# Kernel optimization log

Measured on AMD Instinct MI355X. Metric: run time of the kernel, lower is better.

Reference implementation:

```python
import jax, jax.numpy as jnp
import numpy as np

SIGMA = 0.1
B_PARAM = 1.0
EPS_NORM = 1e-12  # torch F.normalize eps
EPS_MIN = 1e-5


def setup_inputs() -> dict:
    key = jax.random.key(0)
    k1, k2 = jax.random.split(key)
    x = jax.random.normal(k1, (4, 64, 64, 64), dtype=jnp.float32)
    y = jax.random.normal(k2, (4, 64, 64, 64), dtype=jnp.float32)
    return {"x": x, "y": y}


def reference(x, y):
    B, C, H, W = x.shape
    N = H * W
    xf = x.reshape(B, C, N)
    yf = y.reshape(B, C, N)
    # F.normalize along channel dim (L2, eps-clamped denominator)
    xn = xf / jnp.maximum(jnp.linalg.norm(xf, axis=1, keepdims=True), EPS_NORM)
    yn = yf / jnp.maximum(jnp.linalg.norm(yf, axis=1, keepdims=True), EPS_NORM)
    xt = jnp.transpose(xn, (0, 2, 1))  # [B, N, C]
    yt = jnp.transpose(yn, (0, 2, 1))  # [B, N, C]
    x2 = jnp.sum(xt * xt, axis=-1, keepdims=True)          # [B, N, 1]
    y2 = jnp.sum(yt * yt, axis=-1)[:, None, :]             # [B, 1, N]
    d2 = x2 + y2 - 2.0 * jnp.einsum('bnc,bmc->bnm', xt, yt)  # [B, N, N]
    dist = jnp.sqrt(jnp.maximum(d2, 0.0))
    d_min = jnp.min(dist, axis=-1, keepdims=True)
    d_scaled = dist / (d_min + EPS_MIN)
    w = jnp.exp((B_PARAM - d_scaled) / SIGMA)
    cx = w / jnp.sum(w, axis=-1, keepdims=True)
    cx_max = jnp.max(cx, axis=-1)  # [B, N]
    return -jnp.log(jnp.mean(cx_max + EPS_MIN))
```

## Files before the change

### kernel.cpp

```cpp
#include <hip/hip_runtime.h>
#include <math.h>

constexpr int B_   = 4;
constexpr int C_   = 64;
constexpr int HW   = 4096;
constexpr int ROWS = B_ * HW;

constexpr float SIGMA    = 0.1f;
constexpr float EPS_MIN  = 1e-5f;
constexpr float EPS_NORM = 1e-12f;
constexpr float LOG2E    = 1.44269504088896340736f;

constexpr int XR  = 64;
constexpr int NW  = 16;
constexpr int YW  = HW / NW;
constexpr int SRW = 32;
constexpr int NSW = YW / SRW;

using short8  = __attribute__((ext_vector_type(8))) short;
using floatx4 = __attribute__((ext_vector_type(4))) float;

__device__ inline ushort f2bf(float f) {
    unsigned u = __float_as_uint(f);
    unsigned r = u + 0x7FFFu + ((u >> 16) & 1u);
    return (ushort)(r >> 16);
}

__global__ __launch_bounds__(256) void nrm_kernel(const float* __restrict__ x,
                                                  const float* __restrict__ y,
                                                  ushort* __restrict__ xn,
                                                  ushort* __restrict__ yn,
                                                  float* __restrict__ total) {
    int p = blockIdx.x * 256 + threadIdx.x;
    if (p == 0) *total = 0.0f;
    const float* src; ushort* dst; int q; float sgn;
    if (p < ROWS) { src = x; dst = xn; q = p; sgn = -2.0f; }
    else          { src = y; dst = yn; q = p - ROWS; sgn = 1.0f; }
    int b = q >> 12;
    int n = q & (HW - 1);
    const float* base = src + ((size_t)b * C_) * HW + n;
    float v[C_];
    float ss = 0.0f;
#pragma unroll
    for (int c = 0; c < C_; ++c) {
        v[c] = base[(size_t)c * HW];
        ss = fmaf(v[c], v[c], ss);
    }
    float scale = sgn / fmaxf(sqrtf(ss), EPS_NORM);
    short8* o = (short8*)(dst + (size_t)q * C_);
#pragma unroll
    for (int c8 = 0; c8 < C_ / 8; ++c8) {
        short8 pk;
#pragma unroll
        for (int j = 0; j < 8; ++j) pk[j] = (short)f2bf(v[c8 * 8 + j] * scale);
        o[c8] = pk;
    }
}

__global__ __launch_bounds__(1024, 4) void main_kernel(const ushort* __restrict__ xn,
                                                       const ushort* __restrict__ yn,
                                                       float* __restrict__ total) {
    __shared__ short8 stg[NW][2][SRW * 8];
    __shared__ float  red[NW][XR];
    __shared__ float  dmf[XR];

    const int tid  = threadIdx.x;
    const int wid  = tid >> 6;
    const int lane = tid & 63;
    const int lrow = lane & 15;
    const int kgrp = lane >> 4;

    const int blk   = blockIdx.x;
    const int b     = blk >> 6;
    const int nbase = (blk & 63) * XR;

    const ushort* xb = xn + (size_t)(b * HW + nbase) * C_;
    short8 xf0[4], xf1[4];
#pragma unroll
    for (int xt = 0; xt < 4; ++xt) {
        xf0[xt] = *(const short8*)(xb + (xt * 16 + lrow) * C_ + kgrp * 8);
        xf1[xt] = *(const short8*)(xb + (xt * 16 + lrow) * C_ + 32 + kgrp * 8);
    }

    const short8* yq = (const short8*)(yn + (size_t)(b * HW + wid * YW) * C_);
    const int wbase = (lane >> 3) * 8 + ((lane & 7) ^ (lane >> 3));

    short8 v[4];
    float m2[4] = {INFINITY, INFINITY, INFINITY, INFINITY};

#pragma unroll
    for (int g = 0; g < 4; ++g) v[g] = yq[g * 64 + lane];
#pragma unroll
    for (int g = 0; g < 4; ++g) stg[wid][0][g * 64 + wbase] = v[g];

    for (int s = 0; s < NSW; ++s) {
        int cur = s & 1;
        if (s + 1 < NSW) {
#pragma unroll
            for (int g = 0; g < 4; ++g) v[g] = yq[(s + 1) * 256 + g * 64 + lane];
        }
#pragma unroll
        for (int yt = 0; yt < 2; ++yt) {
            int p = yt * 16 + lrow, q = p & 7;
            short8 ya0 = stg[wid][cur][p * 8 + (kgrp ^ q)];
            short8 ya1 = stg[wid][cur][p * 8 + ((kgrp + 4) ^ q)];
#pragma unroll
            for (int xt = 0; xt < 4; ++xt) {
                floatx4 acc = {2.0f, 2.0f, 2.0f, 2.0f};
                acc = __builtin_amdgcn_mfma_f32_16x16x32_bf16(ya0, xf0[xt], acc, 0, 0, 0);
                acc = __builtin_amdgcn_mfma_f32_16x16x32_bf16(ya1, xf1[xt], acc, 0, 0, 0);
                m2[xt] = fminf(m2[xt],
                         fminf(fminf(acc[0], acc[1]), fminf(acc[2], acc[3])));
            }
        }
        if (s + 1 < NSW) {
#pragma unroll
            for (int g = 0; g < 4; ++g) stg[wid][cur ^ 1][g * 64 + wbase] = v[g];
        }
    }

#pragma unroll
    for (int off = 16; off < 64; off <<= 1)
#pragma unroll
        for (int xt = 0; xt < 4; ++xt)
            m2[xt] = fminf(m2[xt], __shfl_xor(m2[xt], off));
    if (kgrp == 0)
#pragma unroll
        for (int xt = 0; xt < 4; ++xt) red[wid][xt * 16 + lrow] = m2[xt];
    __syncthreads();
    if (tid < XR) {
        float m = red[0][tid];
#pragma unroll
        for (int w = 1; w < NW; ++w) m = fminf(m, red[w][tid]);
        dmf[tid] = sqrtf(fmaxf(m, 0.0f));
    }
    __syncthreads();

    float kk2[4], c02[4];
#pragma unroll
    for (int xt = 0; xt < 4; ++xt) {
        float dm = dmf[xt * 16 + lrow];
        kk2[xt] = LOG2E / (SIGMA * (dm + EPS_MIN));
        c02[xt] = dm * kk2[xt];
    }

    float s2[4] = {0.0f, 0.0f, 0.0f, 0.0f};
#pragma unroll
    for (int g = 0; g < 4; ++g) v[g] = yq[g * 64 + lane];
#pragma unroll
    for (int g = 0; g < 4; ++g) stg[wid][0][g * 64 + wbase] = v[g];

    for (int s = 0; s < NSW; ++s) {
        int cur = s & 1;
        if (s + 1 < NSW) {
#pragma unroll
            for (int g = 0; g < 4; ++g) v[g] = yq[(s + 1) * 256 + g * 64 + lane];
        }
#pragma unroll
        for (int yt = 0; yt < 2; ++yt) {
            int p = yt * 16 + lrow, q = p & 7;
            short8 ya0 = stg[wid][cur][p * 8 + (kgrp ^ q)];
            short8 ya1 = stg[wid][cur][p * 8 + ((kgrp + 4) ^ q)];
#pragma unroll
            for (int xt = 0; xt < 4; ++xt) {
                floatx4 acc = {2.0f, 2.0f, 2.0f, 2.0f};
                acc = __builtin_amdgcn_mfma_f32_16x16x32_bf16(ya0, xf0[xt], acc, 0, 0, 0);
                acc = __builtin_amdgcn_mfma_f32_16x16x32_bf16(ya1, xf1[xt], acc, 0, 0, 0);
#pragma unroll
                for (int r = 0; r < 4; ++r) {
                    float d = __builtin_amdgcn_sqrtf(acc[r]);
                    s2[xt] += __builtin_amdgcn_exp2f(fmaf(-kk2[xt], d, c02[xt]));
                }
            }
        }
        if (s + 1 < NSW) {
#pragma unroll
            for (int g = 0; g < 4; ++g) stg[wid][cur ^ 1][g * 64 + wbase] = v[g];
        }
    }

#pragma unroll
    for (int off = 16; off < 64; off <<= 1)
#pragma unroll
        for (int xt = 0; xt < 4; ++xt)
            s2[xt] += __shfl_xor(s2[xt], off);
    if (kgrp == 0)
#pragma unroll
        for (int xt = 0; xt < 4; ++xt) red[wid][xt * 16 + lrow] = s2[xt];
    __syncthreads();

    if (tid < 64) {
        float Ssum = red[0][tid];
#pragma unroll
        for (int w = 1; w < NW; ++w) Ssum += red[w][tid];
        float acc = __builtin_amdgcn_rcpf(Ssum) + EPS_MIN;
#pragma unroll
        for (int off = 32; off > 0; off >>= 1) acc += __shfl_down(acc, off);
        if (tid == 0) atomicAdd(total, acc);
    }
}

__global__ void final_kernel(const float* __restrict__ total,
                             float* __restrict__ out) {
    out[0] = -logf(total[0] / (float)ROWS);
}

extern "C" void kernel_launch(void* const* d_in, const int* in_sizes, int n_in,
                              void* d_out, int out_size, void* d_ws, size_t ws_size,
                              hipStream_t stream) {
    const float* x = (const float*)d_in[0];
    const float* y = (const float*)d_in[1];
    float* out = (float*)d_out;

    char* ws = (char*)d_ws;
    size_t nrm_bytes = (size_t)ROWS * C_ * sizeof(ushort);
    ushort* xn    = (ushort*)(ws);
    ushort* yn    = (ushort*)(ws + nrm_bytes);
    float*  total = (float*)(ws + 2 * nrm_bytes);

    hipLaunchKernelGGL(nrm_kernel, dim3(2 * ROWS / 256), dim3(256), 0, stream,
                       x, y, xn, yn, total);
    hipLaunchKernelGGL(main_kernel, dim3(ROWS / XR), dim3(1024), 0, stream,
                       xn, yn, total);
    hipLaunchKernelGGL(final_kernel, dim3(1), dim3(1), 0, stream, total, out);
}
```

Baseline: 93.29 us.

## Fuse normalize, distance and final kernels into one cooperative launch

Merges the normalization, main distance/softmax pass and final log into a single cooperative kernel separated by grid-wide syncs, removing two kernel launches and their gaps. Normalization is respread so 8 threads share one row, with a shuffle reduction of the sum of squares. The min and exp accumulations are lightly reordered. It relies on all 256 blocks of 1024 threads being co-resident, and grid.sync adds its own barrier cost.

```diff
diff --git a/kernel.cpp b/kernel.cpp
--- a/kernel.cpp
+++ b/kernel.cpp
@@ -1,5 +1,8 @@
 #include <hip/hip_runtime.h>
+#include <hip/hip_cooperative_groups.h>
 #include <math.h>
+
+namespace cg = cooperative_groups;
 
 constexpr int B_   = 4;
 constexpr int C_   = 64;
@@ -26,40 +29,10 @@
     return (ushort)(r >> 16);
 }
 
-__global__ __launch_bounds__(256) void nrm_kernel(const float* __restrict__ x,
-                                                  const float* __restrict__ y,
-                                                  ushort* __restrict__ xn,
-                                                  ushort* __restrict__ yn,
-                                                  float* __restrict__ total) {
-    int p = blockIdx.x * 256 + threadIdx.x;
-    if (p == 0) *total = 0.0f;
-    const float* src; ushort* dst; int q; float sgn;
-    if (p < ROWS) { src = x; dst = xn; q = p; sgn = -2.0f; }
-    else          { src = y; dst = yn; q = p - ROWS; sgn = 1.0f; }
-    int b = q >> 12;
-    int n = q & (HW - 1);
-    const float* base = src + ((size_t)b * C_) * HW + n;
-    float v[C_];
-    float ss = 0.0f;
-#pragma unroll
-    for (int c = 0; c < C_; ++c) {
-        v[c] = base[(size_t)c * HW];
-        ss = fmaf(v[c], v[c], ss);
-    }
-    float scale = sgn / fmaxf(sqrtf(ss), EPS_NORM);
-    short8* o = (short8*)(dst + (size_t)q * C_);
-#pragma unroll
-    for (int c8 = 0; c8 < C_ / 8; ++c8) {
-        short8 pk;
-#pragma unroll
-        for (int j = 0; j < 8; ++j) pk[j] = (short)f2bf(v[c8 * 8 + j] * scale);
-        o[c8] = pk;
-    }
-}
-
-__global__ __launch_bounds__(1024, 4) void main_kernel(const ushort* __restrict__ xn,
-                                                       const ushort* __restrict__ yn,
-                                                       float* __restrict__ total) {
+__global__ __launch_bounds__(1024, 4)
+void fused_kernel(const float* __restrict__ x, const float* __restrict__ y,
+                  ushort* __restrict__ xn, ushort* __restrict__ yn,
+                  float* __restrict__ total, float* __restrict__ out) {
     __shared__ short8 stg[NW][2][SRW * 8];
     __shared__ float  red[NW][XR];
     __shared__ float  dmf[XR];
@@ -69,8 +42,38 @@
     const int lane = tid & 63;
     const int lrow = lane & 15;
     const int kgrp = lane >> 4;
-
-    const int blk   = blockIdx.x;
+    const int blk  = blockIdx.x;
+
+    cg::grid_group grid = cg::this_grid();
+
+    {
+        int g   = blk * 1024 + tid;
+        int p   = g >> 3;
+        int oct = g & 7;
+        if (g == 0) *total = 0.0f;
+        const float* src; ushort* dst; int q; float sgn;
+        if (p < ROWS) { src = x; dst = xn; q = p; sgn = -2.0f; }
+        else          { src = y; dst = yn; q = p - ROWS; sgn = 1.0f; }
+        int b = q >> 12;
+        int n = q & (HW - 1);
+        const float* base = src + (size_t)(b * C_) * HW + n;
+        float v[8];
+        float ss = 0.0f;
+#pragma unroll
+        for (int j = 0; j < 8; ++j) {
+            v[j] = base[(oct * 8 + j) * HW];
+            ss = fmaf(v[j], v[j], ss);
+        }
+#pragma unroll
+        for (int o = 1; o < 8; o <<= 1) ss += __shfl_xor(ss, o);
+        float scale = sgn / fmaxf(sqrtf(ss), EPS_NORM);
+        short8 pk;
+#pragma unroll
+        for (int j = 0; j < 8; ++j) pk[j] = (short)f2bf(v[j] * scale);
+        ((short8*)(dst + (size_t)q * C_))[oct] = pk;
+    }
+    grid.sync();
+
     const int b     = blk >> 6;
     const int nbase = (blk & 63) * XR;
 
@@ -109,8 +112,8 @@
                 floatx4 acc = {2.0f, 2.0f, 2.0f, 2.0f};
                 acc = __builtin_amdgcn_mfma_f32_16x16x32_bf16(ya0, xf0[xt], acc, 0, 0, 0);
                 acc = __builtin_amdgcn_mfma_f32_16x16x32_bf16(ya1, xf1[xt], acc, 0, 0, 0);
-                m2[xt] = fminf(m2[xt],
-                         fminf(fminf(acc[0], acc[1]), fminf(acc[2], acc[3])));
+                m2[xt] = fminf(fminf(fminf(acc[0], acc[1]), acc[2]),
+                               fminf(acc[3], m2[xt]));
             }
         }
         if (s + 1 < NSW) {
@@ -166,11 +169,14 @@
                 floatx4 acc = {2.0f, 2.0f, 2.0f, 2.0f};
                 acc = __builtin_amdgcn_mfma_f32_16x16x32_bf16(ya0, xf0[xt], acc, 0, 0, 0);
                 acc = __builtin_amdgcn_mfma_f32_16x16x32_bf16(ya1, xf1[xt], acc, 0, 0, 0);
-#pragma unroll
-                for (int r = 0; r < 4; ++r) {
-                    float d = __builtin_amdgcn_sqrtf(acc[r]);
-                    s2[xt] += __builtin_amdgcn_exp2f(fmaf(-kk2[xt], d, c02[xt]));
-                }
+                float d0 = __builtin_amdgcn_sqrtf(acc[0]);
+                float d1 = __builtin_amdgcn_sqrtf(acc[1]);
+                float d2 = __builtin_amdgcn_sqrtf(acc[2]);
+                float d3 = __builtin_amdgcn_sqrtf(acc[3]);
+                s2[xt] += __builtin_amdgcn_exp2f(fmaf(-kk2[xt], d0, c02[xt]));
+                s2[xt] += __builtin_amdgcn_exp2f(fmaf(-kk2[xt], d1, c02[xt]));
+                s2[xt] += __builtin_amdgcn_exp2f(fmaf(-kk2[xt], d2, c02[xt]));
+                s2[xt] += __builtin_amdgcn_exp2f(fmaf(-kk2[xt], d3, c02[xt]));
             }
         }
         if (s + 1 < NSW) {
@@ -198,11 +204,9 @@
         for (int off = 32; off > 0; off >>= 1) acc += __shfl_down(acc, off);
         if (tid == 0) atomicAdd(total, acc);
     }
-}
-
-__global__ void final_kernel(const float* __restrict__ total,
-                             float* __restrict__ out) {
-    out[0] = -logf(total[0] / (float)ROWS);
+
+    grid.sync();
+    if (blk == 0 && tid == 0) out[0] = -logf(total[0] / (float)ROWS);
 }
 
 extern "C" void kernel_launch(void* const* d_in, const int* in_sizes, int n_in,
@@ -218,9 +222,8 @@
     ushort* yn    = (ushort*)(ws + nrm_bytes);
     float*  total = (float*)(ws + 2 * nrm_bytes);
 
-    hipLaunchKernelGGL(nrm_kernel, dim3(2 * ROWS / 256), dim3(256), 0, stream,
-                       x, y, xn, yn, total);
-    hipLaunchKernelGGL(main_kernel, dim3(ROWS / XR), dim3(1024), 0, stream,
-                       xn, yn, total);
-    hipLaunchKernelGGL(final_kernel, dim3(1), dim3(1), 0, stream, total, out);
+    void* args[] = { (void*)&x, (void*)&y, (void*)&xn, (void*)&yn,
+                     (void*)&total, (void*)&out };
+    hipLaunchCooperativeKernel((const void*)fused_kernel, dim3(256), dim3(1024),
+                               args, 0, stream);
 }
```

Measured after the change: 148.6 us. 1.59x slower.

## Load Y tiles straight into LDS and fuse the final reduction kernel

Applied to the files above, without the earlier changes.

The y-tile staging now uses global_load_lds to copy 16-byte chunks straight from global memory into each wave's LDS double buffer, ordered by vmcnt waits. This replaces the register round trip and the ds_write. The XOR bank swizzle moves into the normalization kernel's store, so the raw copy still lands in conflict-free order. The separate single-thread final kernel is removed: the last block, found with an atomic counter, computes the log. This saves one launch but adds a threadfence and atomic tail to every block.

```diff
diff --git a/kernel.cpp b/kernel.cpp
--- a/kernel.cpp
+++ b/kernel.cpp
@@ -5,6 +5,7 @@
 constexpr int C_   = 64;
 constexpr int HW   = 4096;
 constexpr int ROWS = B_ * HW;
+constexpr int GRID = 256;
 
 constexpr float SIGMA    = 0.1f;
 constexpr float EPS_MIN  = 1e-5f;
@@ -26,19 +27,28 @@
     return (ushort)(r >> 16);
 }
 
+__device__ inline void gload16(const ushort* g, void* lds) {
+    __builtin_amdgcn_global_load_lds(
+        (const __attribute__((address_space(1))) void*)g,
+        (__attribute__((address_space(3))) void*)lds, 16, 0, 0);
+}
+
+#define WAIT_VMCNT(n) asm volatile("s_waitcnt vmcnt(" #n ")" ::: "memory")
+
 __global__ __launch_bounds__(256) void nrm_kernel(const float* __restrict__ x,
                                                   const float* __restrict__ y,
                                                   ushort* __restrict__ xn,
                                                   ushort* __restrict__ yn,
-                                                  float* __restrict__ total) {
+                                                  float* __restrict__ total,
+                                                  unsigned* __restrict__ cnt) {
     int p = blockIdx.x * 256 + threadIdx.x;
-    if (p == 0) *total = 0.0f;
-    const float* src; ushort* dst; int q; float sgn;
-    if (p < ROWS) { src = x; dst = xn; q = p; sgn = -2.0f; }
-    else          { src = y; dst = yn; q = p - ROWS; sgn = 1.0f; }
+    if (p == 0) { *total = 0.0f; *cnt = 0u; }
+    const float* src; ushort* dst; int q; float sgn; bool isy;
+    if (p < ROWS) { src = x; dst = xn; q = p; sgn = -2.0f; isy = false; }
+    else          { src = y; dst = yn; q = p - ROWS; sgn = 1.0f; isy = true; }
     int b = q >> 12;
     int n = q & (HW - 1);
-    const float* base = src + ((size_t)b * C_) * HW + n;
+    const float* base = src + (size_t)(b * C_) * HW + n;
     float v[C_];
     float ss = 0.0f;
 #pragma unroll
@@ -48,18 +58,21 @@
     }
     float scale = sgn / fmaxf(sqrtf(ss), EPS_NORM);
     short8* o = (short8*)(dst + (size_t)q * C_);
+    int sw = isy ? (n & 7) : 0;
 #pragma unroll
     for (int c8 = 0; c8 < C_ / 8; ++c8) {
         short8 pk;
 #pragma unroll
         for (int j = 0; j < 8; ++j) pk[j] = (short)f2bf(v[c8 * 8 + j] * scale);
-        o[c8] = pk;
+        o[c8 ^ sw] = pk;
     }
 }
 
 __global__ __launch_bounds__(1024, 4) void main_kernel(const ushort* __restrict__ xn,
                                                        const ushort* __restrict__ yn,
-                                                       float* __restrict__ total) {
+                                                       float* __restrict__ total,
+                                                       unsigned* __restrict__ cnt,
+                                                       float* __restrict__ out) {
     __shared__ short8 stg[NW][2][SRW * 8];
     __shared__ float  red[NW][XR];
     __shared__ float  dmf[XR];
@@ -82,23 +95,23 @@
         xf1[xt] = *(const short8*)(xb + (xt * 16 + lrow) * C_ + 32 + kgrp * 8);
     }
 
-    const short8* yq = (const short8*)(yn + (size_t)(b * HW + wid * YW) * C_);
-    const int wbase = (lane >> 3) * 8 + ((lane & 7) ^ (lane >> 3));
-
-    short8 v[4];
+    const ushort* yb = yn + (size_t)(b * HW + wid * YW) * C_ + lane * 8;
+
+#define ISSUE(s, buf) do {                                              \
+        const ushort* gp_ = yb + (size_t)(s) * SRW * C_;                \
+        _Pragma("unroll")                                               \
+        for (int g_ = 0; g_ < 4; ++g_)                                  \
+            gload16(gp_ + g_ * 64 * 8, (void*)&stg[wid][buf][g_ * 64]); \
+    } while (0)
+
     float m2[4] = {INFINITY, INFINITY, INFINITY, INFINITY};
 
-#pragma unroll
-    for (int g = 0; g < 4; ++g) v[g] = yq[g * 64 + lane];
-#pragma unroll
-    for (int g = 0; g < 4; ++g) stg[wid][0][g * 64 + wbase] = v[g];
-
+    ISSUE(0, 0);
     for (int s = 0; s < NSW; ++s) {
         int cur = s & 1;
-        if (s + 1 < NSW) {
-#pragma unroll
-            for (int g = 0; g < 4; ++g) v[g] = yq[(s + 1) * 256 + g * 64 + lane];
-        }
+        if (s + 1 < NSW) { ISSUE(s + 1, cur ^ 1); WAIT_VMCNT(4); }
+        else             { WAIT_VMCNT(0); }
+        __builtin_amdgcn_sched_barrier(0);
 #pragma unroll
         for (int yt = 0; yt < 2; ++yt) {
             int p = yt * 16 + lrow, q = p & 7;
@@ -109,13 +122,9 @@
                 floatx4 acc = {2.0f, 2.0f, 2.0f, 2.0f};
                 acc = __builtin_amdgcn_mfma_f32_16x16x32_bf16(ya0, xf0[xt], acc, 0, 0, 0);
                 acc = __builtin_amdgcn_mfma_f32_16x16x32_bf16(ya1, xf1[xt], acc, 0, 0, 0);
-                m2[xt] = fminf(m2[xt],
-                         fminf(fminf(acc[0], acc[1]), fminf(acc[2], acc[3])));
+                m2[xt] = fminf(fminf(fminf(acc[0], acc[1]), acc[2]),
+                               fminf(acc[3], m2[xt]));
             }
-        }
-        if (s + 1 < NSW) {
-#pragma unroll
-            for (int g = 0; g < 4; ++g) stg[wid][cur ^ 1][g * 64 + wbase] = v[g];
         }
     }
 
@@ -145,17 +154,12 @@
     }
 
     float s2[4] = {0.0f, 0.0f, 0.0f, 0.0f};
-#pragma unroll
-    for (int g = 0; g < 4; ++g) v[g] = yq[g * 64 + lane];
-#pragma unroll
-    for (int g = 0; g < 4; ++g) stg[wid][0][g * 64 + wbase] = v[g];
-
+    ISSUE(0, 0);
     for (int s = 0; s < NSW; ++s) {
         int cur = s & 1;
-        if (s + 1 < NSW) {
-#pragma unroll
-            for (int g = 0; g < 4; ++g) v[g] = yq[(s + 1) * 256 + g * 64 + lane];
-        }
+        if (s + 1 < NSW) { ISSUE(s + 1, cur ^ 1); WAIT_VMCNT(4); }
+        else             { WAIT_VMCNT(0); }
+        __builtin_amdgcn_sched_barrier(0);
 #pragma unroll
         for (int yt = 0; yt < 2; ++yt) {
             int p = yt * 16 + lrow, q = p & 7;
@@ -166,18 +170,18 @@
                 floatx4 acc = {2.0f, 2.0f, 2.0f, 2.0f};
                 acc = __builtin_amdgcn_mfma_f32_16x16x32_bf16(ya0, xf0[xt], acc, 0, 0, 0);
                 acc = __builtin_amdgcn_mfma_f32_16x16x32_bf16(ya1, xf1[xt], acc, 0, 0, 0);
-#pragma unroll
-                for (int r = 0; r < 4; ++r) {
-                    float d = __builtin_amdgcn_sqrtf(acc[r]);
-                    s2[xt] += __builtin_amdgcn_exp2f(fmaf(-kk2[xt], d, c02[xt]));
-                }
+                float d0 = __builtin_amdgcn_sqrtf(acc[0]);
+                float d1 = __builtin_amdgcn_sqrtf(acc[1]);
+                float d2 = __builtin_amdgcn_sqrtf(acc[2]);
+                float d3 = __builtin_amdgcn_sqrtf(acc[3]);
+                s2[xt] += __builtin_amdgcn_exp2f(fmaf(-kk2[xt], d0, c02[xt]));
+                s2[xt] += __builtin_amdgcn_exp2f(fmaf(-kk2[xt], d1, c02[xt]));
+                s2[xt] += __builtin_amdgcn_exp2f(fmaf(-kk2[xt], d2, c02[xt]));
+                s2[xt] += __builtin_amdgcn_exp2f(fmaf(-kk2[xt], d3, c02[xt]));
             }
         }
-        if (s + 1 < NSW) {
-#pragma unroll
-            for (int g = 0; g < 4; ++g) stg[wid][cur ^ 1][g * 64 + wbase] = v[g];
-        }
-    }
+    }
+#undef ISSUE
 
 #pragma unroll
     for (int off = 16; off < 64; off <<= 1)
@@ -190,19 +194,24 @@
     __syncthreads();
 
     if (tid < 64) {
-        float Ssum = red[0][tid];
-#pragma unroll
-        for (int w = 1; w < NW; ++w) Ssum += red[w][tid];
-        float acc = __builtin_amdgcn_rcpf(Ssum) + EPS_MIN;
+        float Ssum = (tid < XR) ? red[0][tid] : 0.0f;
+        if (tid < XR)
+#pragma unroll
+            for (int w = 1; w < NW; ++w) Ssum += red[w][tid];
+        float acc = (tid < XR) ? (__builtin_amdgcn_rcpf(Ssum) + EPS_MIN) : 0.0f;
 #pragma unroll
         for (int off = 32; off > 0; off >>= 1) acc += __shfl_down(acc, off);
-        if (tid == 0) atomicAdd(total, acc);
-    }
-}
-
-__global__ void final_kernel(const float* __restrict__ total,
-                             float* __restrict__ out) {
-    out[0] = -logf(total[0] / (float)ROWS);
+        if (tid == 0) {
+            atomicAdd(total, acc);
+            __threadfence();
+            unsigned done = atomicAdd(cnt, 1u);
+            if (done == GRID - 1) {
+                __threadfence();
+                float t = atomicAdd(total, 0.0f);
+                out[0] = -logf(t / (float)ROWS);
+            }
+        }
+    }
 }
 
 extern "C" void kernel_launch(void* const* d_in, const int* in_sizes, int n_in,
@@ -214,13 +223,13 @@
 
     char* ws = (char*)d_ws;
     size_t nrm_bytes = (size_t)ROWS * C_ * sizeof(ushort);
-    ushort* xn    = (ushort*)(ws);
-    ushort* yn    = (ushort*)(ws + nrm_bytes);
-    float*  total = (float*)(ws + 2 * nrm_bytes);
+    ushort*   xn    = (ushort*)(ws);
+    ushort*   yn    = (ushort*)(ws + nrm_bytes);
+    float*    total = (float*)(ws + 2 * nrm_bytes);
+    unsigned* cnt   = (unsigned*)(ws + 2 * nrm_bytes + 16);
 
     hipLaunchKernelGGL(nrm_kernel, dim3(2 * ROWS / 256), dim3(256), 0, stream,
-                       x, y, xn, yn, total);
-    hipLaunchKernelGGL(main_kernel, dim3(ROWS / XR), dim3(1024), 0, stream,
-                       xn, yn, total);
-    hipLaunchKernelGGL(final_kernel, dim3(1), dim3(1), 0, stream, total, out);
-}
+                       x, y, xn, yn, total, cnt);
+    hipLaunchKernelGGL(main_kernel, dim3(GRID), dim3(1024), 0, stream,
+                       xn, yn, total, cnt, out);
+}
```

Result: slower. 95.27 us (+2.1%).
